# Performance work log

Measured on AMD Instinct MI355X. Metric: run time of the kernel, lower is better.

The kernel has to match this reference:

```python
import jax, jax.numpy as jnp
import numpy as np

B, C, H, W = 16, 256, 128, 128  # H must equal W for this module's dilation trick to be consistent
K = 2  # kernel_size (lifting taps)


def setup_inputs() -> dict:
    key = jax.random.key(0)
    ks = jax.random.split(key, 6)
    C4 = C // 4
    return {
        "x": jax.random.normal(ks[0], (B, C, H, W), jnp.float32),
        "conv1x1_w": jax.random.normal(ks[1], (C, C), jnp.float32) / np.sqrt(C).astype(np.float32),
        "lp_v": jax.random.uniform(ks[2], (C4, 1, K, 1), jnp.float32),  # low_pass_filter_v
        "hp_v": jax.random.uniform(ks[3], (C4, 1, K, 1), jnp.float32),  # high_pass_filter_v
        "lp_h": jax.random.uniform(ks[4], (C4, 1, 1, K), jnp.float32),  # low_pass_filter_h
        "hp_h": jax.random.uniform(ks[5], (C4, 1, 1, K), jnp.float32),  # high_pass_filter_h
    }


def _interleave(e, o, axis):
    # interleave e/o along `axis`: out[..., 2i, ...] = e[..., i, ...], out[..., 2i+1, ...] = o[..., i, ...]
    s = jnp.stack([e, o], axis=axis + 1)
    sh = list(e.shape)
    sh[axis] *= 2
    return s.reshape(sh)


def reference(x, conv1x1_w, lp_v, hp_v, lp_h, hp_h):
    # 1x1 conv (no bias)
    x = jnp.einsum('bchw,oc->bohw', x, conv1x1_w)
    b_, c_, h_, w_ = x.shape
    # pad_mode == 'discard': crop to multiple of kernel_size
    x = x[:, :, :h_ - h_ % K, :w_ - w_ % K]
    c4 = c_ // 4
    a = x[:, :c4]
    bq = x[:, c4:2 * c4]
    cq = x[:, 2 * c4:3 * c4]
    dq = x[:, 3 * c4:]
    # per-channel 2-tap combos: w0 * first_half + w1 * second_half
    lv0 = lp_v[:, 0, 0, 0][None, :, None, None]; lv1 = lp_v[:, 0, 1, 0][None, :, None, None]
    hv0 = hp_v[:, 0, 0, 0][None, :, None, None]; hv1 = hp_v[:, 0, 1, 0][None, :, None, None]
    lh0 = lp_h[:, 0, 0, 0][None, :, None, None]; lh1 = lp_h[:, 0, 0, 1][None, :, None, None]
    hh0 = hp_h[:, 0, 0, 0][None, :, None, None]; hh1 = hp_h[:, 0, 0, 1][None, :, None, None]
    # vertical lifting + row interleave -> [B, C/4, 2H, W]
    x_l = _interleave(lv0 * a + lv1 * bq, hv0 * a + hv1 * bq, 2)
    x_h = _interleave(lv0 * cq + lv1 * dq, hv0 * cq + hv1 * dq, 2)
    # horizontal lifting (valid because H == W) + column interleave -> [B, C/4, 2H, 2W]
    x_e = lh0 * x_l + lh1 * x_h
    x_o = hh0 * x_l + hh1 * x_h
    return _interleave(x_e, x_o, 3)
```

## Files before the change

kernel.cpp:

```cpp
#include <hip/hip_runtime.h>

#define HW 16384

typedef __attribute__((ext_vector_type(8))) __bf16 bf16x8;
typedef __attribute__((ext_vector_type(4))) float floatx4;
typedef __attribute__((ext_vector_type(8))) unsigned short ushort8_t;

typedef const __attribute__((address_space(1))) unsigned int gu32;
typedef __attribute__((address_space(3))) unsigned int lu32;

__device__ __forceinline__ unsigned short f2bf(float f) {
    unsigned int u = __builtin_bit_cast(unsigned int, f);
    unsigned int r = (u + 0x7FFFu + ((u >> 16) & 1u)) >> 16;
    return (unsigned short)r;
}

__device__ __forceinline__ void gload_lds16(const unsigned short* g, unsigned short* l) {
    __builtin_amdgcn_global_load_lds((gu32*)g, (lu32*)l, 16, 0, 0);
}

__global__ void wconv_kernel(const float* __restrict__ w, unsigned short* __restrict__ wb) {
    int i = blockIdx.x * 256 + threadIdx.x;
    int row = i >> 8, c = i & 255;
    int kt = c >> 6, kl = c & 63;
    int idx = (row * 64 + kl) ^ ((row & 7) << 3);
    wb[kt * 16384 + idx] = f2bf(w[i]);
}

__global__ __launch_bounds__(512, 4) void fused_gemm_lift(
        const float* __restrict__ x,
        const unsigned short* __restrict__ wb,
        const float* __restrict__ lp_v,
        const float* __restrict__ hp_v,
        const float* __restrict__ lp_h,
        const float* __restrict__ hp_h,
        float* __restrict__ out) {
    __shared__ alignas(16) unsigned short wbuf_s[2][16384];
    __shared__ alignas(16) unsigned short xbuf_s[8192];

    const int tid  = threadIdx.x;
    const int wv   = tid >> 6;
    const int lane = tid & 63;
    const int mgrp  = wv & 3;
    const int nhalf = wv >> 2;
    const int tile = blockIdx.x & 127;
    const int bb   = blockIdx.x >> 7;
    const int p0   = tile * 128;

    const float* xb = x + (size_t)bb * 256 * HW;

    const int lrow  = lane & 15;
    const int khalf = lane >> 4;
    const int fswz  = (lrow & 7) << 3;

    const int px  = tid & 127;
    const int cb  = (tid >> 7) * 16;
    const int xw0 = (px * 64 + cb) ^ ((px & 7) << 3);
    const int xw1 = (px * 64 + cb + 8) ^ ((px & 7) << 3);

    floatx4 acc[4][4];
    #pragma unroll
    for (int g = 0; g < 4; ++g)
        #pragma unroll
        for (int n = 0; n < 4; ++n) {
            floatx4 z = {0.f, 0.f, 0.f, 0.f};
            acc[g][n] = z;
        }

    float xv[16];

    {
        const float* xs = xb + (size_t)cb * HW + p0 + px;
        #pragma unroll
        for (int j = 0; j < 16; ++j) xv[j] = xs[(size_t)j * HW];
        #pragma unroll
        for (int pass = 0; pass < 4; ++pass) {
            int ch = pass * 512 + wv * 64;
            gload_lds16(wb + (size_t)(ch + lane) * 8, &wbuf_s[0][ch * 8]);
        }
        ushort8_t v0, v1;
        #pragma unroll
        for (int j = 0; j < 8; ++j) { v0[j] = f2bf(xv[j]); v1[j] = f2bf(xv[8 + j]); }
        *reinterpret_cast<ushort8_t*>(&xbuf_s[xw0]) = v0;
        *reinterpret_cast<ushort8_t*>(&xbuf_s[xw1]) = v1;
    }
    __syncthreads();

    for (int kt = 0; kt < 4; ++kt) {
        const int cw = kt & 1;

        if (kt < 3) {
            const float* xs = xb + (size_t)((kt + 1) * 64 + cb) * HW + p0 + px;
            #pragma unroll
            for (int j = 0; j < 16; ++j) xv[j] = xs[(size_t)j * HW];
            #pragma unroll
            for (int pass = 0; pass < 4; ++pass) {
                int ch = pass * 512 + wv * 64;
                gload_lds16(wb + (size_t)((kt + 1) * 16384) + (size_t)(ch + lane) * 8,
                            &wbuf_s[cw ^ 1][ch * 8]);
            }
        }

        #pragma unroll
        for (int kc = 0; kc < 2; ++kc) {
            bf16x8 af[4], bfr[4];
            #pragma unroll
            for (int g = 0; g < 4; ++g)
                af[g] = *reinterpret_cast<const bf16x8*>(
                    &wbuf_s[cw][((g * 64 + mgrp * 16 + lrow) * 64 + kc * 32 + khalf * 8) ^ fswz]);
            #pragma unroll
            for (int n = 0; n < 4; ++n)
                bfr[n] = *reinterpret_cast<const bf16x8*>(
                    &xbuf_s[((nhalf * 64 + n * 16 + lrow) * 64 + kc * 32 + khalf * 8) ^ fswz]);
            #pragma unroll
            for (int g = 0; g < 4; ++g)
                #pragma unroll
                for (int n = 0; n < 4; ++n)
                    acc[g][n] = __builtin_amdgcn_mfma_f32_16x16x32_bf16(af[g], bfr[n], acc[g][n], 0, 0, 0);
        }

        if (kt < 3) {
            __syncthreads();
            ushort8_t v0, v1;
            #pragma unroll
            for (int j = 0; j < 8; ++j) { v0[j] = f2bf(xv[j]); v1[j] = f2bf(xv[8 + j]); }
            *reinterpret_cast<ushort8_t*>(&xbuf_s[xw0]) = v0;
            *reinterpret_cast<ushort8_t*>(&xbuf_s[xw1]) = v1;
            __syncthreads();
        }
    }

    const int lgr = lane >> 4;
    #pragma unroll
    for (int ri = 0; ri < 4; ++ri) {
        const int q = mgrp * 16 + lgr * 4 + ri;
        const float lv0 = lp_v[2 * q], lv1 = lp_v[2 * q + 1];
        const float hv0 = hp_v[2 * q], hv1 = hp_v[2 * q + 1];
        const float lh0 = lp_h[2 * q], lh1 = lp_h[2 * q + 1];
        const float hh0 = hp_h[2 * q], hh1 = hp_h[2 * q + 1];
        float* outq = out + (size_t)(bb * 64 + q) * 65536;
        #pragma unroll
        for (int n = 0; n < 4; ++n) {
            const int p = p0 + nhalf * 64 + n * 16 + lrow;
            const int h = p >> 7;
            const int w = p & 127;
            const float a  = acc[0][n][ri];
            const float b2 = acc[1][n][ri];
            const float c2 = acc[2][n][ri];
            const float d2 = acc[3][n][ri];
            const float xl0 = lv0 * a + lv1 * b2;
            const float xl1 = hv0 * a + hv1 * b2;
            const float xh0 = lv0 * c2 + lv1 * d2;
            const float xh1 = hv0 * c2 + hv1 * d2;
            float2 r0 = make_float2(lh0 * xl0 + lh1 * xh0, hh0 * xl0 + hh1 * xh0);
            float2 r1 = make_float2(lh0 * xl1 + lh1 * xh1, hh0 * xl1 + hh1 * xh1);
            *reinterpret_cast<float2*>(outq + (size_t)(2 * h) * 256 + 2 * w)     = r0;
            *reinterpret_cast<float2*>(outq + (size_t)(2 * h + 1) * 256 + 2 * w) = r1;
        }
    }
}

extern "C" void kernel_launch(void* const* d_in, const int* in_sizes, int n_in,
                              void* d_out, int out_size, void* d_ws, size_t ws_size,
                              hipStream_t stream) {
    const float* x   = (const float*)d_in[0];
    const float* w   = (const float*)d_in[1];
    const float* lpv = (const float*)d_in[2];
    const float* hpv = (const float*)d_in[3];
    const float* lph = (const float*)d_in[4];
    const float* hph = (const float*)d_in[5];
    float* outp = (float*)d_out;
    unsigned short* wbp = (unsigned short*)d_ws;

    wconv_kernel<<<dim3(256), dim3(256), 0, stream>>>(w, wbp);
    fused_gemm_lift<<<dim3(2048), dim3(512), 0, stream>>>(x, wbp, lpv, hpv, lph, hph, outp);
}
```

Before: 132.5 us.

## Load activations straight into MFMA B-fragments, drop the LDS x staging and halve the pixel tile

Each lane now loads its activation values from global memory directly in the register layout the MFMA B operand expects and converts them to bf16 in registers. This removes the x shared-memory buffer and one of the two barriers per K step. The pixel tile per block shrinks from 128 to 64, so twice as many blocks are launched and each wave covers 16 pixels by 128 output channels. In exchange the full weight tile is re-staged into LDS for every half-size tile, doubling weight traffic, and the per-lane global loads are less coalesced (16-pixel runs).

```diff
diff --git a/kernel.cpp b/kernel.cpp
--- a/kernel.cpp
+++ b/kernel.cpp
@@ -36,118 +36,105 @@
         const float* __restrict__ hp_h,
         float* __restrict__ out) {
     __shared__ alignas(16) unsigned short wbuf_s[2][16384];
-    __shared__ alignas(16) unsigned short xbuf_s[8192];
 
     const int tid  = threadIdx.x;
     const int wv   = tid >> 6;
     const int lane = tid & 63;
-    const int mgrp  = wv & 3;
-    const int nhalf = wv >> 2;
-    const int tile = blockIdx.x & 127;
-    const int bb   = blockIdx.x >> 7;
-    const int p0   = tile * 128;
+    const int nt   = wv >> 1;
+    const int mh   = wv & 1;
+    const int tile = blockIdx.x & 255;
+    const int bb   = blockIdx.x >> 8;
+    const int p0   = tile * 64;
+
+    const int lrow = lane & 15;
+    const int kh   = lane >> 4;
+    const int fswz = (lrow & 7) << 3;
 
     const float* xb = x + (size_t)bb * 256 * HW;
+    const float* xp = xb + p0 + nt * 16 + lrow;
 
-    const int lrow  = lane & 15;
-    const int khalf = lane >> 4;
-    const int fswz  = (lrow & 7) << 3;
-
-    const int px  = tid & 127;
-    const int cb  = (tid >> 7) * 16;
-    const int xw0 = (px * 64 + cb) ^ ((px & 7) << 3);
-    const int xw1 = (px * 64 + cb + 8) ^ ((px & 7) << 3);
-
-    floatx4 acc[4][4];
+    floatx4 acc[2][4];
     #pragma unroll
-    for (int g = 0; g < 4; ++g)
+    for (int s = 0; s < 2; ++s)
         #pragma unroll
-        for (int n = 0; n < 4; ++n) {
+        for (int g = 0; g < 4; ++g) {
             floatx4 z = {0.f, 0.f, 0.f, 0.f};
-            acc[g][n] = z;
+            acc[s][g] = z;
         }
 
-    float xv[16];
+    float xf[2][16];
 
-    {
-        const float* xs = xb + (size_t)cb * HW + p0 + px;
-        #pragma unroll
-        for (int j = 0; j < 16; ++j) xv[j] = xs[(size_t)j * HW];
-        #pragma unroll
-        for (int pass = 0; pass < 4; ++pass) {
-            int ch = pass * 512 + wv * 64;
-            gload_lds16(wb + (size_t)(ch + lane) * 8, &wbuf_s[0][ch * 8]);
-        }
-        ushort8_t v0, v1;
-        #pragma unroll
-        for (int j = 0; j < 8; ++j) { v0[j] = f2bf(xv[j]); v1[j] = f2bf(xv[8 + j]); }
-        *reinterpret_cast<ushort8_t*>(&xbuf_s[xw0]) = v0;
-        *reinterpret_cast<ushort8_t*>(&xbuf_s[xw1]) = v1;
+    #pragma unroll
+    for (int pass = 0; pass < 4; ++pass) {
+        int ch = pass * 512 + wv * 64;
+        gload_lds16(wb + (size_t)(ch + lane) * 8, &wbuf_s[0][ch * 8]);
+    }
+    #pragma unroll
+    for (int jj = 0; jj < 16; ++jj) {
+        int ch = (jj >> 3) * 32 + kh * 8 + (jj & 7);
+        xf[0][jj] = xp[(size_t)ch * HW];
     }
     __syncthreads();
 
+    #pragma unroll
     for (int kt = 0; kt < 4; ++kt) {
         const int cw = kt & 1;
 
         if (kt < 3) {
-            const float* xs = xb + (size_t)((kt + 1) * 64 + cb) * HW + p0 + px;
-            #pragma unroll
-            for (int j = 0; j < 16; ++j) xv[j] = xs[(size_t)j * HW];
             #pragma unroll
             for (int pass = 0; pass < 4; ++pass) {
                 int ch = pass * 512 + wv * 64;
-                gload_lds16(wb + (size_t)((kt + 1) * 16384) + (size_t)(ch + lane) * 8,
+                gload_lds16(wb + (size_t)(kt + 1) * 16384 + (size_t)(ch + lane) * 8,
                             &wbuf_s[cw ^ 1][ch * 8]);
+            }
+            #pragma unroll
+            for (int jj = 0; jj < 16; ++jj) {
+                int ch = (kt + 1) * 64 + (jj >> 3) * 32 + kh * 8 + (jj & 7);
+                xf[cw ^ 1][jj] = xp[(size_t)ch * HW];
             }
         }
 
         #pragma unroll
         for (int kc = 0; kc < 2; ++kc) {
-            bf16x8 af[4], bfr[4];
+            ushort8_t u;
             #pragma unroll
-            for (int g = 0; g < 4; ++g)
-                af[g] = *reinterpret_cast<const bf16x8*>(
-                    &wbuf_s[cw][((g * 64 + mgrp * 16 + lrow) * 64 + kc * 32 + khalf * 8) ^ fswz]);
+            for (int j = 0; j < 8; ++j) u[j] = f2bf(xf[cw][kc * 8 + j]);
+            const bf16x8 bfv = __builtin_bit_cast(bf16x8, u);
             #pragma unroll
-            for (int n = 0; n < 4; ++n)
-                bfr[n] = *reinterpret_cast<const bf16x8*>(
-                    &xbuf_s[((nhalf * 64 + n * 16 + lrow) * 64 + kc * 32 + khalf * 8) ^ fswz]);
-            #pragma unroll
-            for (int g = 0; g < 4; ++g)
+            for (int s = 0; s < 2; ++s) {
+                bf16x8 af[4];
                 #pragma unroll
-                for (int n = 0; n < 4; ++n)
-                    acc[g][n] = __builtin_amdgcn_mfma_f32_16x16x32_bf16(af[g], bfr[n], acc[g][n], 0, 0, 0);
+                for (int g = 0; g < 4; ++g) {
+                    int row = g * 64 + (mh * 2 + s) * 16 + lrow;
+                    af[g] = *reinterpret_cast<const bf16x8*>(
+                        &wbuf_s[cw][(row * 64 + kc * 32 + kh * 8) ^ fswz]);
+                }
+                #pragma unroll
+                for (int g = 0; g < 4; ++g)
+                    acc[s][g] = __builtin_amdgcn_mfma_f32_16x16x32_bf16(af[g], bfv, acc[s][g], 0, 0, 0);
+            }
         }
 
-        if (kt < 3) {
-            __syncthreads();
-            ushort8_t v0, v1;
-            #pragma unroll
-            for (int j = 0; j < 8; ++j) { v0[j] = f2bf(xv[j]); v1[j] = f2bf(xv[8 + j]); }
-            *reinterpret_cast<ushort8_t*>(&xbuf_s[xw0]) = v0;
-            *reinterpret_cast<ushort8_t*>(&xbuf_s[xw1]) = v1;
-            __syncthreads();
-        }
+        if (kt < 3) __syncthreads();
     }
 
-    const int lgr = lane >> 4;
+    const int px = p0 + nt * 16 + lrow;
+    const int h  = px >> 7;
+    const int w  = px & 127;
     #pragma unroll
-    for (int ri = 0; ri < 4; ++ri) {
-        const int q = mgrp * 16 + lgr * 4 + ri;
-        const float lv0 = lp_v[2 * q], lv1 = lp_v[2 * q + 1];
-        const float hv0 = hp_v[2 * q], hv1 = hp_v[2 * q + 1];
-        const float lh0 = lp_h[2 * q], lh1 = lp_h[2 * q + 1];
-        const float hh0 = hp_h[2 * q], hh1 = hp_h[2 * q + 1];
-        float* outq = out + (size_t)(bb * 64 + q) * 65536;
+    for (int s = 0; s < 2; ++s)
         #pragma unroll
-        for (int n = 0; n < 4; ++n) {
-            const int p = p0 + nhalf * 64 + n * 16 + lrow;
-            const int h = p >> 7;
-            const int w = p & 127;
-            const float a  = acc[0][n][ri];
-            const float b2 = acc[1][n][ri];
-            const float c2 = acc[2][n][ri];
-            const float d2 = acc[3][n][ri];
+        for (int ri = 0; ri < 4; ++ri) {
+            const int q = (mh * 2 + s) * 16 + kh * 4 + ri;
+            const float lv0 = lp_v[2 * q], lv1 = lp_v[2 * q + 1];
+            const float hv0 = hp_v[2 * q], hv1 = hp_v[2 * q + 1];
+            const float lh0 = lp_h[2 * q], lh1 = lp_h[2 * q + 1];
+            const float hh0 = hp_h[2 * q], hh1 = hp_h[2 * q + 1];
+            float* outq = out + (size_t)(bb * 64 + q) * 65536;
+            const float a  = acc[s][0][ri];
+            const float b2 = acc[s][1][ri];
+            const float c2 = acc[s][2][ri];
+            const float d2 = acc[s][3][ri];
             const float xl0 = lv0 * a + lv1 * b2;
             const float xl1 = hv0 * a + hv1 * b2;
             const float xh0 = lv0 * c2 + lv1 * d2;
@@ -157,7 +144,6 @@
             *reinterpret_cast<float2*>(outq + (size_t)(2 * h) * 256 + 2 * w)     = r0;
             *reinterpret_cast<float2*>(outq + (size_t)(2 * h + 1) * 256 + 2 * w) = r1;
         }
-    }
 }
 
 extern "C" void kernel_launch(void* const* d_in, const int* in_sizes, int n_in,
@@ -173,5 +159,5 @@
     unsigned short* wbp = (unsigned short*)d_ws;
 
     wconv_kernel<<<dim3(256), dim3(256), 0, stream>>>(w, wbp);
-    fused_gemm_lift<<<dim3(2048), dim3(512), 0, stream>>>(x, wbp, lpv, hpv, lph, hph, outp);
+    fused_gemm_lift<<<dim3(4096), dim3(512), 0, stream>>>(x, wbp, lpv, hpv, lph, hph, outp);
 }
```

Measured after the change: 139.8 us. +5.5%, slower.
